# Optimization experiments

Hardware: AMD Instinct MI355X
Metric: run time of the kernel (lower is better)

## Reference

```python
import jax, jax.numpy as jnp
from jax import lax
import numpy as np

PADDING = 1
STRIDE = 1


def setup_inputs() -> dict:
    key = jax.random.key(0)
    k1, k2 = jax.random.split(key)
    x = jax.random.normal(k1, (256, 224, 224), dtype=jnp.float32)       # [C, H, W]
    kernel = jax.random.normal(k2, (256, 256, 3, 3), dtype=jnp.float32)  # [O, C, kh, kw]
    return {"x": x, "kernel": kernel}


def reference(x, kernel):
    # Direct conv2d with zero padding and stride, equivalent to the
    # nested-loop torch implementation (cross-correlation, no bias).
    out = lax.conv_general_dilated(
        x[None],                      # [1, C, H, W]
        kernel,                       # [O, C, kh, kw]
        window_strides=(STRIDE, STRIDE),
        padding=[(PADDING, PADDING), (PADDING, PADDING)],
        dimension_numbers=("NCHW", "OIHW", "NCHW"),
    )
    return out[0]                     # [O, Hout, Wout]
```

## Files before the change

### kernel.cpp

```cpp
#include <hip/hip_runtime.h>
#include <hip/hip_bf16.h>
#include <stdint.h>

#define C_IN  256
#define C_OUT 256
#define H_IN  224
#define W_IN  224
#define HP    226
#define WP    226
#define NPIX  (H_IN * W_IN)
#define BM    256
#define BN    256
#define BK    64

typedef __attribute__((ext_vector_type(8))) short short8;
typedef __attribute__((ext_vector_type(4))) float f32x4;

__device__ __forceinline__ unsigned short f2bf(float f) {
    __hip_bfloat16 b = __float2bfloat16(f);
    return *(unsigned short*)&b;
}

__device__ __forceinline__ void gl_lds16(const unsigned short* g, unsigned short* l) {
    __builtin_amdgcn_global_load_lds(
        (const __attribute__((address_space(1))) unsigned int*)g,
        (__attribute__((address_space(3))) unsigned int*)l,
        16, 0, 0);
}

__global__ void prep_all(const float* __restrict__ x, const float* __restrict__ wk,
                         unsigned short* __restrict__ xp, unsigned short* __restrict__ wb) {
    int b = blockIdx.x;
    int t = threadIdx.x;
    if (b < 3584) {
        int ct = b & 3, wt = (b >> 2) & 3, h = b >> 4;
        int c0 = ct * 64, w0 = wt * 64;
        __shared__ float tile[64][65];
        int w   = t & 63;
        int cl0 = t >> 6;
        #pragma unroll
        for (int i = 0; i < 16; ++i) {
            int cl = i * 4 + cl0;
            float v = 0.f;
            if (w0 + w < W_IN)
                v = x[(size_t)(c0 + cl) * NPIX + (size_t)h * W_IN + w0 + w];
            tile[cl][w] = v;
        }
        __syncthreads();
        int wc = t >> 2;
        int cc = (t & 3) * 16;
        if (w0 + wc < W_IN) {
            uint32_t pk[8];
            #pragma unroll
            for (int j = 0; j < 8; ++j) {
                unsigned short lo = f2bf(tile[cc + 2 * j][wc]);
                unsigned short hi = f2bf(tile[cc + 2 * j + 1][wc]);
                pk[j] = (uint32_t)lo | ((uint32_t)hi << 16);
            }
            size_t base = ((size_t)(h + 1) * WP + (w0 + wc + 1)) * C_IN + c0 + cc;
            uint4* dst = (uint4*)(xp + base);
            dst[0] = make_uint4(pk[0], pk[1], pk[2], pk[3]);
            dst[1] = make_uint4(pk[4], pk[5], pk[6], pk[7]);
        }
        return;
    }
    if (b < 5888) {
        int idx = (b - 3584) * 256 + t;
        int c = idx & 255, o = (idx >> 8) & 255, p = idx >> 16;
        wb[((size_t)p * 256 + o) * 256 + c] = f2bf(wk[((size_t)o * 256 + c) * 9 + p]);
        return;
    }
    int i = (b - 5888) * 256 + t;
    uint4 z = make_uint4(0u, 0u, 0u, 0u);
    if (i < 7232) {
        ((uint4*)xp)[i] = z;
    } else if (i < 14464) {
        ((uint4*)(xp + (size_t)225 * WP * C_IN))[i - 7232] = z;
    } else if (i < 21632) {
        int j = i - 14464; int h = 1 + (j >> 5); int c4 = j & 31;
        ((uint4*)(xp + ((size_t)h * WP) * C_IN))[c4] = z;
    } else if (i < 28800) {
        int j = i - 21632; int h = 1 + (j >> 5); int c4 = j & 31;
        ((uint4*)(xp + ((size_t)h * WP + 225) * C_IN))[c4] = z;
    }
}


__launch_bounds__(512, 2)
__global__ void conv_gemm(const unsigned short* __restrict__ xp,
                          const unsigned short* __restrict__ wb,
                          float* __restrict__ out) {
    int bid = blockIdx.x;
    int xcd = bid & 7, orig = bid >> 3;
    int nt = (xcd < 4 ? xcd * 25 : 100 + (xcd - 4) * 24) + orig;
    int n0 = nt * BN;
    int t  = threadIdx.x;
    int l  = t & 63, wv = t >> 6;

    __shared__ __align__(16) unsigned short lds[2 * 32768];

    int q8 = ((l & 7) ^ (l >> 3)) * 8;
    int rA = l >> 3;
    int rowLo = 16 * wv + rA;
    int rowHi = rowLo + 8;
    int offA00 = rowLo * C_IN + q8;
    int offA01 = rowHi * C_IN + q8;
    int offA10 = (128 + rowLo) * C_IN + q8;
    int offA11 = (128 + rowHi) * C_IN + q8;
    int offB00, offB01, offB10, offB11;
    {
        int nc;
        nc = n0 + rowLo;       { int h_ = nc / W_IN; offB00 = (h_ * WP + nc - h_ * W_IN) * C_IN + q8; }
        nc = n0 + rowHi;       { int h_ = nc / W_IN; offB01 = (h_ * WP + nc - h_ * W_IN) * C_IN + q8; }
        nc = n0 + 128 + rowLo; { int h_ = nc / W_IN; offB10 = (h_ * WP + nc - h_ * W_IN) * C_IN + q8; }
        nc = n0 + 128 + rowHi; { int h_ = nc / W_IN; offB11 = (h_ * WP + nc - h_ * W_IN) * C_IN + q8; }
    }

    int la = l & 15;
    int lk = l >> 4;
    int wr = wv >> 2;
    int wc = wv & 3;
    int mo = wr * 128;
    int no = wc * 64;
    int xq0 = (lk ^ (la & 7)) * 8;
    int xq1 = ((4 + lk) ^ (la & 7)) * 8;

    f32x4 acc[8][4];
    #pragma unroll
    for (int i = 0; i < 8; ++i)
        #pragma unroll
        for (int j = 0; j < 4; ++j)
            acc[i][j] = f32x4{0.f, 0.f, 0.f, 0.f};

#define STAGEH(BD, S, H) do {                                                \
    int s_ = (S), p_ = s_ >> 2, cs_ = (s_ & 3) << 6;                         \
    if ((H) < 2) {                                                           \
        const unsigned short* g_ = wb + p_ * 65536 + cs_;                    \
        unsigned short* d_ = &lds[(BD) * 32768 + (H) * 8192 + wv * 1024];    \
        gl_lds16(g_ + ((H) ? offA10 : offA00), d_);                          \
        gl_lds16(g_ + ((H) ? offA11 : offA01), d_ + 512);                    \
    } else {                                                                 \
        int kh_ = (p_ * 11) >> 5, kw_ = p_ - 3 * kh_;                        \
        const unsigned short* g_ = xp + (kh_ * WP + kw_) * C_IN + cs_;       \
        unsigned short* d_ = &lds[(BD) * 32768 + 16384 + ((H) - 2) * 8192 + wv * 1024]; \
        gl_lds16(g_ + ((H) == 3 ? offB10 : offB00), d_);                     \
        gl_lds16(g_ + ((H) == 3 ? offB11 : offB01), d_ + 512);               \
    }                                                                        \
} while (0)

#define MFMAG(AF, BF, GOFF) do {                                             \
    __builtin_amdgcn_s_setprio(1);                                           \
    _Pragma("unroll")                                                        \
    for (int i_ = 0; i_ < 4; ++i_)                                           \
        _Pragma("unroll")                                                    \
        for (int j_ = 0; j_ < 4; ++j_)                                       \
            acc[(GOFF) + i_][j_] = __builtin_amdgcn_mfma_f32_16x16x32_bf16(  \
                AF[i_], BF[j_], acc[(GOFF) + i_][j_], 0, 0, 0);              \
    __builtin_amdgcn_s_setprio(0);                                           \
} while (0)

#define HALF(BC, SS, DO_STAGE, VMSTR) do {                                   \
    if (DO_STAGE) STAGEH(1 ^ (BC), SS, 0);                                   \
    asm volatile("s_waitcnt " VMSTR ::: "memory");                           \
    __builtin_amdgcn_sched_barrier(0);                                       \
    __builtin_amdgcn_s_barrier();                                            \
    __builtin_amdgcn_sched_barrier(0);                                       \
    short8 bf0_[4], bf1_[4], a_[4];                                          \
    _Pragma("unroll")                                                        \
    for (int j_ = 0; j_ < 4; ++j_)                                           \
        bf0_[j_] = *(const short8*)&lds[(BC) * 32768 + 16384 + (no + j_ * 16 + la) * BK + xq0]; \
    _Pragma("unroll")                                                        \
    for (int i_ = 0; i_ < 4; ++i_)                                           \
        a_[i_] = *(const short8*)&lds[(BC) * 32768 + (mo + i_ * 16 + la) * BK + xq0]; \
    MFMAG(a_, bf0_, 0);                                                      \
    if (DO_STAGE) STAGEH(1 ^ (BC), SS, 1);                                   \
    _Pragma("unroll")                                                        \
    for (int i_ = 0; i_ < 4; ++i_)                                           \
        a_[i_] = *(const short8*)&lds[(BC) * 32768 + (mo + 64 + i_ * 16 + la) * BK + xq0]; \
    MFMAG(a_, bf0_, 4);                                                      \
    if (DO_STAGE) STAGEH(1 ^ (BC), SS, 2);                                   \
    _Pragma("unroll")                                                        \
    for (int j_ = 0; j_ < 4; ++j_)                                           \
        bf1_[j_] = *(const short8*)&lds[(BC) * 32768 + 16384 + (no + j_ * 16 + la) * BK + xq1]; \
    _Pragma("unroll")                                                        \
    for (int i_ = 0; i_ < 4; ++i_)                                           \
        a_[i_] = *(const short8*)&lds[(BC) * 32768 + (mo + i_ * 16 + la) * BK + xq1]; \
    MFMAG(a_, bf1_, 0);                                                      \
    if (DO_STAGE) STAGEH(1 ^ (BC), SS, 3);                                   \
    _Pragma("unroll")                                                        \
    for (int i_ = 0; i_ < 4; ++i_)                                           \
        a_[i_] = *(const short8*)&lds[(BC) * 32768 + (mo + 64 + i_ * 16 + la) * BK + xq1]; \
    MFMAG(a_, bf1_, 4);                                                      \
    asm volatile("s_waitcnt lgkmcnt(0)" ::: "memory");                       \
    __builtin_amdgcn_sched_barrier(0);                                       \
    __builtin_amdgcn_s_barrier();                                            \
    __builtin_amdgcn_sched_barrier(0);                                       \
} while (0)

    STAGEH(0, 0, 0); STAGEH(0, 0, 1); STAGEH(0, 0, 2); STAGEH(0, 0, 3);
    #pragma unroll 1
    for (int k = 0; k < 17; ++k) {
        HALF(0, 2 * k + 1, 1, "vmcnt(2)");
        HALF(1, 2 * k + 2, 1, "vmcnt(2)");
    }
    HALF(0, 35, 1, "vmcnt(2)");
    HALF(1, 0, 0, "vmcnt(0)");

#undef HALF
#undef MFMAG
#undef STAGEH

    int ro = lk * 4;
    #pragma unroll
    for (int i = 0; i < 8; ++i) {
        #pragma unroll
        for (int j = 0; j < 4; ++j) {
            int oo = mo + i * 16 + ro;
            int nn = n0 + no + j * 16 + la;
            #pragma unroll
            for (int r = 0; r < 4; ++r)
                out[(size_t)(oo + r) * NPIX + nn] = acc[i][j][r];
        }
    }
}

__global__ void conv_naive(const float* __restrict__ x, const float* __restrict__ wk,
                           float* __restrict__ out) {
    int idx = blockIdx.x * 256 + threadIdx.x;
    int n = idx % NPIX;
    int o = idx / NPIX;
    int h = n / W_IN, w = n - (n / W_IN) * W_IN;
    float s = 0.f;
    for (int c = 0; c < C_IN; ++c) {
        const float* xc = x + (size_t)c * NPIX;
        const float* wc = wk + ((size_t)o * C_IN + c) * 9;
        #pragma unroll
        for (int kh = 0; kh < 3; ++kh) {
            int hh = h + kh - 1;
            if (hh < 0 || hh >= H_IN) continue;
            #pragma unroll
            for (int kw = 0; kw < 3; ++kw) {
                int ww = w + kw - 1;
                if (ww < 0 || ww >= W_IN) continue;
                s += xc[hh * W_IN + ww] * wc[kh * 3 + kw];
            }
        }
    }
    out[idx] = s;
}

extern "C" void kernel_launch(void* const* d_in, const int* in_sizes, int n_in,
                              void* d_out, int out_size, void* d_ws, size_t ws_size,
                              hipStream_t stream) {
    const float* x  = (const float*)d_in[0];
    const float* wk = (const float*)d_in[1];
    float* out = (float*)d_out;

    const size_t xp_elems = (size_t)HP * WP * C_IN;
    const size_t wb_elems = (size_t)9 * 256 * 256;
    const size_t need = (xp_elems + wb_elems) * 2;

    if (ws_size < need) {
        conv_naive<<<(C_OUT * NPIX) / 256, 256, 0, stream>>>(x, wk, out);
        return;
    }

    unsigned short* xp = (unsigned short*)d_ws;
    unsigned short* wb = xp + xp_elems;

    prep_all<<<3584 + 2304 + 113, 256, 0, stream>>>(x, wk, xp, wb);
    conv_gemm<<<196, 512, 0, stream>>>(xp, wb, out);
}
```

Measured before the change: 80.92 us.

## Restructure K-loop into ping-pong style with barriers around each MFMA group

The per-tile pipeline is rewritten so that all four global-to-LDS stage loads for the next tile are issued up front, and each MFMA cluster is wrapped in barrier/waitcnt pairs. This follows a ping-pong schedule where waves in a workgroup alternate between memory and compute phases. The vmcnt wait moves to just before the last MFMA group and loses its partial-count overlap. The change adds many more workgroup barriers per K tile, which can stall waves if they do not actually stagger.

```diff
diff --git a/kernel.cpp b/kernel.cpp
--- a/kernel.cpp
+++ b/kernel.cpp
@@ -148,6 +148,20 @@
     }                                                                        \
 } while (0)
 
+#define PRE() do {                                                           \
+    __builtin_amdgcn_sched_barrier(0);                                       \
+    __builtin_amdgcn_s_barrier();                                            \
+    __builtin_amdgcn_sched_barrier(0);                                       \
+    asm volatile("s_waitcnt lgkmcnt(0)" ::: "memory");                       \
+    __builtin_amdgcn_sched_barrier(0);                                       \
+} while (0)
+
+#define POST() do {                                                          \
+    __builtin_amdgcn_sched_barrier(0);                                       \
+    __builtin_amdgcn_s_barrier();                                            \
+    __builtin_amdgcn_sched_barrier(0);                                       \
+} while (0)
+
 #define MFMAG(AF, BF, GOFF) do {                                             \
     __builtin_amdgcn_s_setprio(1);                                           \
     _Pragma("unroll")                                                        \
@@ -159,55 +173,57 @@
     __builtin_amdgcn_s_setprio(0);                                           \
 } while (0)
 
-#define HALF(BC, SS, DO_STAGE, VMSTR) do {                                   \
-    if (DO_STAGE) STAGEH(1 ^ (BC), SS, 0);                                   \
-    asm volatile("s_waitcnt " VMSTR ::: "memory");                           \
-    __builtin_amdgcn_sched_barrier(0);                                       \
-    __builtin_amdgcn_s_barrier();                                            \
-    __builtin_amdgcn_sched_barrier(0);                                       \
-    short8 bf0_[4], bf1_[4], a_[4];                                          \
+#define KTILE(BC, S2, DO_ST) do {                                            \
+    short8 bf_[4], a_[4];                                                    \
+                                      \
     _Pragma("unroll")                                                        \
     for (int j_ = 0; j_ < 4; ++j_)                                           \
-        bf0_[j_] = *(const short8*)&lds[(BC) * 32768 + 16384 + (no + j_ * 16 + la) * BK + xq0]; \
+        bf_[j_] = *(const short8*)&lds[(BC) * 32768 + 16384 + (no + j_ * 16 + la) * BK + xq0]; \
     _Pragma("unroll")                                                        \
     for (int i_ = 0; i_ < 4; ++i_)                                           \
         a_[i_] = *(const short8*)&lds[(BC) * 32768 + (mo + i_ * 16 + la) * BK + xq0]; \
-    MFMAG(a_, bf0_, 0);                                                      \
-    if (DO_STAGE) STAGEH(1 ^ (BC), SS, 1);                                   \
+    if (DO_ST) { STAGEH((BC) ^ 1, S2, 0); STAGEH((BC) ^ 1, S2, 1);           \
+                 STAGEH((BC) ^ 1, S2, 2); STAGEH((BC) ^ 1, S2, 3); }         \
+    PRE(); MFMAG(a_, bf_, 0); POST();                                        \
+                                                      \
     _Pragma("unroll")                                                        \
     for (int i_ = 0; i_ < 4; ++i_)                                           \
         a_[i_] = *(const short8*)&lds[(BC) * 32768 + (mo + 64 + i_ * 16 + la) * BK + xq0]; \
-    MFMAG(a_, bf0_, 4);                                                      \
-    if (DO_STAGE) STAGEH(1 ^ (BC), SS, 2);                                   \
+    PRE(); MFMAG(a_, bf_, 4); POST();                                        \
+                                                      \
     _Pragma("unroll")                                                        \
     for (int j_ = 0; j_ < 4; ++j_)                                           \
-        bf1_[j_] = *(const short8*)&lds[(BC) * 32768 + 16384 + (no + j_ * 16 + la) * BK + xq1]; \
+        bf_[j_] = *(const short8*)&lds[(BC) * 32768 + 16384 + (no + j_ * 16 + la) * BK + xq1]; \
     _Pragma("unroll")                                                        \
     for (int i_ = 0; i_ < 4; ++i_)                                           \
         a_[i_] = *(const short8*)&lds[(BC) * 32768 + (mo + i_ * 16 + la) * BK + xq1]; \
-    MFMAG(a_, bf1_, 0);                                                      \
-    if (DO_STAGE) STAGEH(1 ^ (BC), SS, 3);                                   \
+    PRE(); MFMAG(a_, bf_, 0); POST();                                        \
+           \
     _Pragma("unroll")                                                        \
     for (int i_ = 0; i_ < 4; ++i_)                                           \
         a_[i_] = *(const short8*)&lds[(BC) * 32768 + (mo + 64 + i_ * 16 + la) * BK + xq1]; \
-    MFMAG(a_, bf1_, 4);                                                      \
-    asm volatile("s_waitcnt lgkmcnt(0)" ::: "memory");                       \
-    __builtin_amdgcn_sched_barrier(0);                                       \
-    __builtin_amdgcn_s_barrier();                                            \
-    __builtin_amdgcn_sched_barrier(0);                                       \
+    asm volatile("s_waitcnt vmcnt(0)" ::: "memory");                         \
+    __builtin_amdgcn_sched_barrier(0);                                       \
+    PRE(); MFMAG(a_, bf_, 4); POST();                                        \
 } while (0)
 
     STAGEH(0, 0, 0); STAGEH(0, 0, 1); STAGEH(0, 0, 2); STAGEH(0, 0, 3);
+    asm volatile("s_waitcnt vmcnt(0)" ::: "memory");
+    __builtin_amdgcn_sched_barrier(0);
+    __builtin_amdgcn_s_barrier();
+    __builtin_amdgcn_sched_barrier(0);
     #pragma unroll 1
     for (int k = 0; k < 17; ++k) {
-        HALF(0, 2 * k + 1, 1, "vmcnt(2)");
-        HALF(1, 2 * k + 2, 1, "vmcnt(2)");
-    }
-    HALF(0, 35, 1, "vmcnt(2)");
-    HALF(1, 0, 0, "vmcnt(0)");
-
-#undef HALF
+        KTILE(0, 2 * k + 1, 1);
+        KTILE(1, 2 * k + 2, 1);
+    }
+    KTILE(0, 35, 1);
+    KTILE(1, 0, 0);
+
+#undef KTILE
 #undef MFMAG
+#undef POST
+#undef PRE
 #undef STAGEH
 
     int ro = lk * 4;
```

Result: slower. 89.75 us (+10.9%).
